# Optimization experiments

Measured on AMD Instinct MI355X. Metric: run time of the kernel, lower is better.

The kernel has to match this reference:

```python
import jax, jax.numpy as jnp
import numpy as np

N_DOMAINS = 8
LN_EPS = 1e-5


def setup_inputs() -> dict:
    key = jax.random.key(0)
    ks = jax.random.split(key, 4)
    N, D_IN, D_HID, D_OUT = 32768, 256, 1024, 256
    x = jax.random.normal(ks[0], (N, D_IN), dtype=jnp.float32)
    domain_types = jax.random.randint(ks[1], (N,), 0, N_DOMAINS, dtype=jnp.int32)
    # Per-domain MLP parameters (8 independent experts)
    W1 = jax.random.normal(ks[2], (N_DOMAINS, D_IN, D_HID), dtype=jnp.float32) * (1.0 / np.sqrt(D_IN))
    b1 = jnp.zeros((N_DOMAINS, D_HID), dtype=jnp.float32)
    gamma = jnp.ones((N_DOMAINS, D_HID), dtype=jnp.float32)
    beta = jnp.zeros((N_DOMAINS, D_HID), dtype=jnp.float32)
    W2 = jax.random.normal(ks[3], (N_DOMAINS, D_HID, D_OUT), dtype=jnp.float32) * (1.0 / np.sqrt(D_HID))
    b2 = jnp.zeros((N_DOMAINS, D_OUT), dtype=jnp.float32)
    return {"x": x, "domain_types": domain_types, "W1": W1, "b1": b1,
            "gamma": gamma, "beta": beta, "W2": W2, "b2": b2}


def _expert_mlp(x, W1d, b1d, gd, bd, W2d, b2d):
    # Linear -> LayerNorm -> ReLU -> (Dropout: identity at eval) -> Linear
    h = x @ W1d + b1d                       # [N, hid]
    mu = jnp.mean(h, axis=-1, keepdims=True)
    var = jnp.mean(jnp.square(h - mu), axis=-1, keepdims=True)
    h = (h - mu) * jax.lax.rsqrt(var + LN_EPS) * gd + bd
    h = jax.nn.relu(h)
    return h @ W2d + b2d                    # [N, out]


def reference(x, domain_types, W1, b1, gamma, beta, W2, b2):
    # output dim == x.shape[-1] (as in the torch code: zeros(batch, x.shape[-1]))
    out = jnp.zeros((x.shape[0], x.shape[-1]), dtype=x.dtype)
    for d in range(N_DOMAINS):  # small fixed expert loop (static MoE dispatch)
        y = _expert_mlp(x, W1[d], b1[d], gamma[d], beta[d], W2[d], b2[d])
        mask = (domain_types == d)[:, None]
        out = jnp.where(mask, y, out)
    return out
```

## Files before the change

### kernel.cpp

```cpp
#include <hip/hip_runtime.h>
#include <hip/hip_bf16.h>


#define ND 8
#define NROWS 32768
#define DIN 256
#define DHID 1024
#define DOUT 256
#define MPAD 33792
#define NTILES 264

typedef short short8 __attribute__((ext_vector_type(8)));
typedef float floatx4 __attribute__((ext_vector_type(4)));

__device__ __forceinline__ unsigned short f2bf(float f) {
    unsigned u = __builtin_bit_cast(unsigned, f);
    unsigned r = u + 0x7fff + ((u >> 16) & 1);
    return (unsigned short)(r >> 16);
}
__device__ __forceinline__ float bf2f(unsigned short h) {
    unsigned u = ((unsigned)h) << 16;
    return __builtin_bit_cast(float, u);
}

#define GLDS16(gp, lp) __builtin_amdgcn_global_load_lds( \
    (const __attribute__((address_space(1))) void*)(gp), \
    (__attribute__((address_space(3))) void*)(lp), 16, 0, 0)

__global__ void transpose_bf16(const float* __restrict__ in,
                               unsigned short* __restrict__ out,
                               int R, int C, int* __restrict__ cnt) {
    __shared__ float t[32][33];
    const int z = blockIdx.z;
    const int c0 = blockIdx.x * 32, r0 = blockIdx.y * 32;
    const int tx = threadIdx.x & 31, ty = threadIdx.x >> 5;
    if (cnt && blockIdx.x == 0 && blockIdx.y == 0 && z == 0 && threadIdx.x < 16)
        cnt[threadIdx.x] = 0;
    const float* src = in + (size_t)z * R * C;
    unsigned short* dst = out + (size_t)z * R * C;
#pragma unroll
    for (int i = 0; i < 32; i += 8)
        t[ty + i][tx] = src[(size_t)(r0 + ty + i) * C + c0 + tx];
    __syncthreads();
#pragma unroll
    for (int i = 0; i < 32; i += 8)
        dst[(size_t)(c0 + ty + i) * R + r0 + tx] = f2bf(t[tx][ty + i]);
}

__global__ void histo(const int* __restrict__ dt, int* __restrict__ counts) {
    __shared__ int lc[ND];
    if (threadIdx.x < ND) lc[threadIdx.x] = 0;
    __syncthreads();
    int i = blockIdx.x * 256 + threadIdx.x;
    atomicAdd(&lc[dt[i]], 1);
    __syncthreads();
    if (threadIdx.x < ND) atomicAdd(&counts[threadIdx.x], lc[threadIdx.x]);
}

__global__ void make_meta(const int* __restrict__ counts, int* __restrict__ cursors,
                          int2* __restrict__ meta, int* __restrict__ perm) {
    if (threadIdx.x == 0 && blockIdx.x == 0) {
        int off = 0, t = 0;
        for (int d = 0; d < ND; d++) {
            cursors[d] = off;
            int nt = (counts[d] + 127) >> 7;
            for (int i = 0; i < nt; i++) meta[t++] = make_int2(d, off + (i << 7));
            for (int p = off + counts[d]; p < off + (nt << 7); p++) perm[p] = -1;
            off += nt << 7;
        }
        for (; t < NTILES; t++) meta[t] = make_int2(-1, 0);
    }
}

__global__ __launch_bounds__(256)
void assign_pos(const int* __restrict__ dt, int* __restrict__ cursors,
                int* __restrict__ perm, int* __restrict__ pos) {
    __shared__ int lcnt[ND];
    __shared__ int lbase[ND];
    const int tid = threadIdx.x;
    if (tid < ND) lcnt[tid] = 0;
    __syncthreads();
    const int r = blockIdx.x * 256 + tid;
    const int d = dt[r];
    const int myrank = atomicAdd(&lcnt[d], 1);
    __syncthreads();
    if (tid < ND && lcnt[tid] > 0)
        lbase[tid] = atomicAdd(&cursors[tid], lcnt[tid]);
    __syncthreads();
    const int p = lbase[d] + myrank;
    pos[r] = p;
    perm[p] = r;
}

__global__ __launch_bounds__(256)
void copy_rows(const float* __restrict__ x, const int* __restrict__ pos,
               unsigned short* __restrict__ xs) {
    const int tid = threadIdx.x;
    const int lane = tid & 63;
    const int r = blockIdx.x * 4 + (tid >> 6);
    const int p = pos[r];
    float4 v = ((const float4*)(x + (size_t)r * DIN))[lane];
    ushort4 o;
    o.x = f2bf(v.x); o.y = f2bf(v.y); o.z = f2bf(v.z); o.w = f2bf(v.w);
    ((ushort4*)(xs + (size_t)p * DIN))[lane] = o;
}

__global__ __launch_bounds__(512, 2)
void gemm_ln(const unsigned short* __restrict__ A,
             const unsigned short* __restrict__ Bt,
             const float* __restrict__ bias,
             const float* __restrict__ gamma,
             const float* __restrict__ beta,
             const int2* __restrict__ meta,
             unsigned short* __restrict__ H) {
    const int2 md = meta[blockIdx.x >> 1];
    const int dom = md.x;
    if (dom < 0) return;
    const int m0 = md.y + (blockIdx.x & 1) * 64;

    __shared__ unsigned short As[64 * 32];
    __shared__ unsigned short Bs[1024 * 32];
    __shared__ float red_s[64][9];
    __shared__ float red_q[64][9];
    __shared__ float mu_s[64], rs_s[64];

    const int tid = threadIdx.x;
    const int lane = tid & 63;
    const int w = tid >> 6;
    const int c16 = lane & 15;
    const int quad = lane >> 4;

    const unsigned short* Abase = A + (size_t)m0 * DIN;
    const unsigned short* Bbase = Bt + (size_t)dom * DHID * DIN;

    floatx4 acc[4][8];
#pragma unroll
    for (int i = 0; i < 4; i++)
#pragma unroll
        for (int j = 0; j < 8; j++) acc[i][j] = 0.f;

    for (int k0 = 0; k0 < DIN; k0 += 32) {
#pragma unroll
        for (int it = 0; it < 8; ++it) {
            const int c = (w * 8 + it) * 64 + lane;
            const int n = c >> 2, kc = c & 3;
            GLDS16(Bbase + (size_t)n * DIN + k0 + kc * 8, &Bs[(w * 8 + it) * 512]);
        }
        if (w < 4) {
            const int c = w * 64 + lane;
            const int m = c >> 2, kc = c & 3;
            GLDS16(Abase + (size_t)m * DIN + k0 + kc * 8, &As[w * 512]);
        }
        __syncthreads();

        const int kk = quad * 8;
        short8 a[4], b[8];
#pragma unroll
        for (int i = 0; i < 4; i++)
            a[i] = *(const short8*)&As[(i * 16 + c16) * 32 + kk];
#pragma unroll
        for (int j = 0; j < 8; j++)
            b[j] = *(const short8*)&Bs[(w * 128 + j * 16 + c16) * 32 + kk];
#pragma unroll
        for (int i = 0; i < 4; i++)
#pragma unroll
            for (int j = 0; j < 8; j++)
                acc[i][j] = __builtin_amdgcn_mfma_f32_16x16x32_bf16(a[i], b[j], acc[i][j], 0, 0, 0);
        __syncthreads();
    }

    float bv[8];
#pragma unroll
    for (int j = 0; j < 8; j++) bv[j] = bias[dom * DHID + w * 128 + j * 16 + c16];

#pragma unroll
    for (int i = 0; i < 4; i++) {
#pragma unroll
        for (int r = 0; r < 4; r++) {
            float s = 0.f, q = 0.f;
#pragma unroll
            for (int j = 0; j < 8; j++) {
                float v = acc[i][j][r] + bv[j];
                acc[i][j][r] = v;
                s += v; q += v * v;
            }
#pragma unroll
            for (int o = 1; o < 16; o <<= 1) {
                s += __shfl_xor(s, o, 64);
                q += __shfl_xor(q, o, 64);
            }
            if (c16 == 0) {
                const int row = i * 16 + quad * 4 + r;
                red_s[row][w] = s;
                red_q[row][w] = q;
            }
        }
    }
    __syncthreads();

    if (tid < 64) {
        float s = 0.f, q = 0.f;
#pragma unroll
        for (int ww = 0; ww < 8; ww++) { s += red_s[tid][ww]; q += red_q[tid][ww]; }
        const float inv = 1.0f / (float)DHID;
        const float mu = s * inv;
        const float var = fmaxf(q * inv - mu * mu, 0.f);
        mu_s[tid] = mu;
        rs_s[tid] = rsqrtf(var + 1e-5f);
    }
    __syncthreads();

    float gv[8], btv[8];
#pragma unroll
    for (int j = 0; j < 8; j++) {
        gv[j] = gamma[dom * DHID + w * 128 + j * 16 + c16];
        btv[j] = beta[dom * DHID + w * 128 + j * 16 + c16];
    }
#pragma unroll
    for (int i = 0; i < 4; i++) {
#pragma unroll
        for (int r = 0; r < 4; r++) {
            const int row = i * 16 + quad * 4 + r;
            const float mu = mu_s[row], rs = rs_s[row];
            unsigned short* hrow = H + (size_t)(m0 + row) * DHID + w * 128;
#pragma unroll
            for (int j = 0; j < 8; j++) {
                float v = (acc[i][j][r] - mu) * rs * gv[j] + btv[j];
                hrow[j * 16 + c16] = f2bf(fmaxf(v, 0.f));
            }
        }
    }
}

__global__ __launch_bounds__(256, 2)
void gemm_bt(const unsigned short* __restrict__ A,
             const unsigned short* __restrict__ Bt,
             const float* __restrict__ bias,
             const int2* __restrict__ meta,
             const int* __restrict__ perm,
             float* __restrict__ Cf,
             const int Ntot, const int K) {
    const int2 md = meta[blockIdx.x];
    const int dom = md.x;
    if (dom < 0) return;
    const int m0 = md.y;
    const int n0 = blockIdx.y * 128;

    __shared__ unsigned short As[128 * 32];
    __shared__ unsigned short Bs[128 * 32];

    const int tid = threadIdx.x;
    const int lane = tid & 63;
    const int w = tid >> 6;
    const int wr = w >> 1, wc = w & 1;

    const unsigned short* Abase = A + (size_t)m0 * K;
    const unsigned short* Bbase = Bt + (size_t)dom * Ntot * K + (size_t)n0 * K;

    floatx4 acc[4][4];
#pragma unroll
    for (int i = 0; i < 4; i++)
#pragma unroll
        for (int j = 0; j < 4; j++) acc[i][j] = 0.f;

    for (int k0 = 0; k0 < K; k0 += 32) {
#pragma unroll
        for (int it = 0; it < 2; ++it) {
            const int c = w * 128 + it * 64 + lane;
            const int m = c >> 2, kc = c & 3;
            GLDS16(Abase + (size_t)m * K + k0 + kc * 8, &As[(w * 128 + it * 64) * 8]);
            GLDS16(Bbase + (size_t)m * K + k0 + kc * 8, &Bs[(w * 128 + it * 64) * 8]);
        }
        __syncthreads();

        short8 a[4], b[4];
        const int kk = (lane >> 4) * 8;
#pragma unroll
        for (int i = 0; i < 4; i++) {
            const int m = wr * 64 + i * 16 + (lane & 15);
            a[i] = *(const short8*)&As[m * 32 + kk];
            const int n = wc * 64 + i * 16 + (lane & 15);
            b[i] = *(const short8*)&Bs[n * 32 + kk];
        }
#pragma unroll
        for (int i = 0; i < 4; i++)
#pragma unroll
            for (int j = 0; j < 4; j++)
                acc[i][j] = __builtin_amdgcn_mfma_f32_16x16x32_bf16(a[i], b[j], acc[i][j], 0, 0, 0);
        __syncthreads();
    }

    const int quad = lane >> 4;
#pragma unroll
    for (int i = 0; i < 4; i++) {
        const int rowbase = m0 + wr * 64 + i * 16 + quad * 4;
#pragma unroll
        for (int r = 0; r < 4; r++) {
            const int orig = perm[rowbase + r];
            if (orig < 0) continue;
#pragma unroll
            for (int j = 0; j < 4; j++) {
                const int col = n0 + wc * 64 + j * 16 + (lane & 15);
                Cf[(size_t)orig * Ntot + col] = acc[i][j][r] + bias[dom * Ntot + col];
            }
        }
    }
}

extern "C" void kernel_launch(void* const* d_in, const int* in_sizes, int n_in,
                              void* d_out, int out_size, void* d_ws, size_t ws_size,
                              hipStream_t stream) {
    const float* x = (const float*)d_in[0];
    const int* dt = (const int*)d_in[1];
    const float* W1 = (const float*)d_in[2];
    const float* b1 = (const float*)d_in[3];
    const float* gamma = (const float*)d_in[4];
    const float* beta = (const float*)d_in[5];
    const float* W2 = (const float*)d_in[6];
    const float* b2 = (const float*)d_in[7];
    float* out = (float*)d_out;

    char* ws = (char*)d_ws;
    size_t off = 0;
    auto take = [&](size_t nbytes) -> char* {
        char* p = ws + off;
        off = (off + nbytes + 255) & ~(size_t)255;
        return p;
    };
    unsigned short* W1T = (unsigned short*)take((size_t)ND * DHID * DIN * 2);
    unsigned short* W2T = (unsigned short*)take((size_t)ND * DOUT * DHID * 2);
    unsigned short* XS  = (unsigned short*)take((size_t)MPAD * DIN * 2);
    unsigned short* H   = (unsigned short*)take((size_t)MPAD * DHID * 2);
    int* PERM   = (int*)take(MPAD * 4);
    int* POS    = (int*)take(NROWS * 4);
    int* CNT    = (int*)take(64);
    int2* META  = (int2*)take(NTILES * 8);
    (void)ws_size; (void)n_in; (void)in_sizes; (void)out_size;

    int* COUNTS = CNT;
    int* CURSORS = CNT + 8;

    transpose_bf16<<<dim3(DHID / 32, DIN / 32, ND), 256, 0, stream>>>(W1, W1T, DIN, DHID, CNT);
    transpose_bf16<<<dim3(DOUT / 32, DHID / 32, ND), 256, 0, stream>>>(W2, W2T, DHID, DOUT, nullptr);
    histo<<<NROWS / 256, 256, 0, stream>>>(dt, COUNTS);
    make_meta<<<1, 1, 0, stream>>>(COUNTS, CURSORS, META, PERM);
    assign_pos<<<NROWS / 256, 256, 0, stream>>>(dt, CURSORS, PERM, POS);
    copy_rows<<<NROWS / 4, 256, 0, stream>>>(x, POS, XS);
    gemm_ln<<<NTILES * 2, 512, 0, stream>>>(XS, W1T, b1, gamma, beta, META, H);
    gemm_bt<<<dim3(NTILES, DOUT / 128), 256, 0, stream>>>(
        H, W2T, b2, META, PERM, out, DOUT, DHID);
}
```

Before: 247.8 us.

## Split LayerNorm: emit partial stats in GEMM1, apply normalization in GEMM2 A-load

The first GEMM used to own full 1024-wide rows (a 64x1024 tile per block with a large LDS B buffer) so it could compute LayerNorm in-block. It now uses standard 128x128 tiles that write pre-norm bf16 H plus per-row partial sums and sums of squares to a stats buffer. The second GEMM reduces those 16 partials per row, then normalizes, applies gamma/beta and ReLU while staging H into LDS. This is meant to give GEMM1 more parallelism and a smaller LDS footprint. In exchange, GEMM2's A path changes from async global-to-LDS loads to register loads with ALU work, and each GEMM2 column block redoes the normalization of the same H rows.

Result: faster. 229.2 us (-7.5%).

```diff
diff --git a/kernel.cpp b/kernel.cpp
--- a/kernel.cpp
+++ b/kernel.cpp
@@ -11,6 +11,7 @@
 #define NTILES 264
 
 typedef short short8 __attribute__((ext_vector_type(8)));
+typedef unsigned short ushort8v __attribute__((ext_vector_type(8)));
 typedef float floatx4 __attribute__((ext_vector_type(4)));
 
 __device__ __forceinline__ unsigned short f2bf(float f) {
@@ -105,83 +106,79 @@
     ((ushort4*)(xs + (size_t)p * DIN))[lane] = o;
 }
 
-__global__ __launch_bounds__(512, 2)
-void gemm_ln(const unsigned short* __restrict__ A,
-             const unsigned short* __restrict__ Bt,
-             const float* __restrict__ bias,
-             const float* __restrict__ gamma,
-             const float* __restrict__ beta,
-             const int2* __restrict__ meta,
-             unsigned short* __restrict__ H) {
-    const int2 md = meta[blockIdx.x >> 1];
+__global__ __launch_bounds__(256, 2)
+void gemm_a(const unsigned short* __restrict__ A,
+            const unsigned short* __restrict__ Bt,
+            const float* __restrict__ bias,
+            const int2* __restrict__ meta,
+            unsigned short* __restrict__ H,
+            float2* __restrict__ stats) {
+    const int2 md = meta[blockIdx.x];
     const int dom = md.x;
     if (dom < 0) return;
-    const int m0 = md.y + (blockIdx.x & 1) * 64;
-
-    __shared__ unsigned short As[64 * 32];
-    __shared__ unsigned short Bs[1024 * 32];
-    __shared__ float red_s[64][9];
-    __shared__ float red_q[64][9];
-    __shared__ float mu_s[64], rs_s[64];
+    const int m0 = md.y;
+    const int n0 = blockIdx.y * 128;
+
+    __shared__ unsigned short As[128 * 32];
+    __shared__ unsigned short Bs[128 * 32];
 
     const int tid = threadIdx.x;
     const int lane = tid & 63;
     const int w = tid >> 6;
-    const int c16 = lane & 15;
-    const int quad = lane >> 4;
+    const int wr = w >> 1, wc = w & 1;
+    const int c16 = lane & 15, quad = lane >> 4;
 
     const unsigned short* Abase = A + (size_t)m0 * DIN;
-    const unsigned short* Bbase = Bt + (size_t)dom * DHID * DIN;
-
-    floatx4 acc[4][8];
+    const unsigned short* Bbase = Bt + (size_t)dom * DHID * DIN + (size_t)n0 * DIN;
+
+    floatx4 acc[4][4];
 #pragma unroll
     for (int i = 0; i < 4; i++)
 #pragma unroll
-        for (int j = 0; j < 8; j++) acc[i][j] = 0.f;
+        for (int j = 0; j < 4; j++) acc[i][j] = 0.f;
 
     for (int k0 = 0; k0 < DIN; k0 += 32) {
 #pragma unroll
-        for (int it = 0; it < 8; ++it) {
-            const int c = (w * 8 + it) * 64 + lane;
-            const int n = c >> 2, kc = c & 3;
-            GLDS16(Bbase + (size_t)n * DIN + k0 + kc * 8, &Bs[(w * 8 + it) * 512]);
-        }
-        if (w < 4) {
-            const int c = w * 64 + lane;
+        for (int it = 0; it < 2; ++it) {
+            const int c = w * 128 + it * 64 + lane;
             const int m = c >> 2, kc = c & 3;
-            GLDS16(Abase + (size_t)m * DIN + k0 + kc * 8, &As[w * 512]);
+            GLDS16(Abase + (size_t)m * DIN + k0 + kc * 8, &As[(w * 128 + it * 64) * 8]);
+            GLDS16(Bbase + (size_t)m * DIN + k0 + kc * 8, &Bs[(w * 128 + it * 64) * 8]);
         }
         __syncthreads();
 
+        short8 a[4], b[4];
         const int kk = quad * 8;
-        short8 a[4], b[8];
+#pragma unroll
+        for (int i = 0; i < 4; i++) {
+            a[i] = *(const short8*)&As[(wr * 64 + i * 16 + c16) * 32 + kk];
+            b[i] = *(const short8*)&Bs[(wc * 64 + i * 16 + c16) * 32 + kk];
+        }
 #pragma unroll
         for (int i = 0; i < 4; i++)
-            a[i] = *(const short8*)&As[(i * 16 + c16) * 32 + kk];
-#pragma unroll
-        for (int j = 0; j < 8; j++)
-            b[j] = *(const short8*)&Bs[(w * 128 + j * 16 + c16) * 32 + kk];
-#pragma unroll
-        for (int i = 0; i < 4; i++)
-#pragma unroll
-            for (int j = 0; j < 8; j++)
+#pragma unroll
+            for (int j = 0; j < 4; j++)
                 acc[i][j] = __builtin_amdgcn_mfma_f32_16x16x32_bf16(a[i], b[j], acc[i][j], 0, 0, 0);
         __syncthreads();
     }
 
-    float bv[8];
-#pragma unroll
-    for (int j = 0; j < 8; j++) bv[j] = bias[dom * DHID + w * 128 + j * 16 + c16];
-
+    float bv[4];
+#pragma unroll
+    for (int j = 0; j < 4; j++)
+        bv[j] = bias[dom * DHID + n0 + wc * 64 + j * 16 + c16];
+
+    float2* st = stats + (size_t)(blockIdx.y * 2 + wc) * MPAD;
 #pragma unroll
     for (int i = 0; i < 4; i++) {
+        const int rowbase = m0 + wr * 64 + i * 16 + quad * 4;
 #pragma unroll
         for (int r = 0; r < 4; r++) {
             float s = 0.f, q = 0.f;
 #pragma unroll
-            for (int j = 0; j < 8; j++) {
-                float v = acc[i][j][r] + bv[j];
-                acc[i][j][r] = v;
+            for (int j = 0; j < 4; j++) {
+                const float v = acc[i][j][r] + bv[j];
+                const int col = n0 + wc * 64 + j * 16 + c16;
+                H[(size_t)(rowbase + r) * DHID + col] = f2bf(v);
                 s += v; q += v * v;
             }
 #pragma unroll
@@ -189,19 +186,44 @@
                 s += __shfl_xor(s, o, 64);
                 q += __shfl_xor(q, o, 64);
             }
-            if (c16 == 0) {
-                const int row = i * 16 + quad * 4 + r;
-                red_s[row][w] = s;
-                red_q[row][w] = q;
-            }
-        }
-    }
-    __syncthreads();
-
-    if (tid < 64) {
+            if (c16 == 0) st[rowbase + r] = make_float2(s, q);
+        }
+    }
+}
+
+__global__ __launch_bounds__(256, 2)
+void gemm_b_ln(const unsigned short* __restrict__ H,
+               const unsigned short* __restrict__ Bt,
+               const float* __restrict__ bias,
+               const float* __restrict__ gamma,
+               const float* __restrict__ beta,
+               const float2* __restrict__ stats,
+               const int2* __restrict__ meta,
+               const int* __restrict__ perm,
+               float* __restrict__ out) {
+    const int2 md = meta[blockIdx.x];
+    const int dom = md.x;
+    if (dom < 0) return;
+    const int m0 = md.y;
+    const int n0 = blockIdx.y * 128;
+
+    __shared__ unsigned short As[128 * 32];
+    __shared__ unsigned short Bs[128 * 32];
+    __shared__ float mu_s[128], rs_s[128];
+
+    const int tid = threadIdx.x;
+    const int lane = tid & 63;
+    const int w = tid >> 6;
+    const int wr = w >> 1, wc = w & 1;
+    const int c16 = lane & 15, quad = lane >> 4;
+
+    if (tid < 128) {
         float s = 0.f, q = 0.f;
 #pragma unroll
-        for (int ww = 0; ww < 8; ww++) { s += red_s[tid][ww]; q += red_q[tid][ww]; }
+        for (int cb = 0; cb < 16; cb++) {
+            const float2 p = stats[(size_t)cb * MPAD + m0 + tid];
+            s += p.x; q += p.y;
+        }
         const float inv = 1.0f / (float)DHID;
         const float mu = s * inv;
         const float var = fmaxf(q * inv - mu * mu, 0.f);
@@ -210,77 +232,52 @@
     }
     __syncthreads();
 
-    float gv[8], btv[8];
-#pragma unroll
-    for (int j = 0; j < 8; j++) {
-        gv[j] = gamma[dom * DHID + w * 128 + j * 16 + c16];
-        btv[j] = beta[dom * DHID + w * 128 + j * 16 + c16];
-    }
-#pragma unroll
-    for (int i = 0; i < 4; i++) {
-#pragma unroll
-        for (int r = 0; r < 4; r++) {
-            const int row = i * 16 + quad * 4 + r;
+    const unsigned short* Hbase = H + (size_t)m0 * DHID;
+    const unsigned short* Bbase = Bt + (size_t)dom * DOUT * DHID + (size_t)n0 * DHID;
+    const float* gbase = gamma + dom * DHID;
+    const float* bbase = beta + dom * DHID;
+
+    floatx4 acc[4][4];
+#pragma unroll
+    for (int i = 0; i < 4; i++)
+#pragma unroll
+        for (int j = 0; j < 4; j++) acc[i][j] = 0.f;
+
+    for (int k0 = 0; k0 < DHID; k0 += 32) {
+#pragma unroll
+        for (int it = 0; it < 2; ++it) {
+            const int c = it * 256 + tid;
+            const int row = c >> 2, kg = c & 3;
             const float mu = mu_s[row], rs = rs_s[row];
-            unsigned short* hrow = H + (size_t)(m0 + row) * DHID + w * 128;
-#pragma unroll
-            for (int j = 0; j < 8; j++) {
-                float v = (acc[i][j][r] - mu) * rs * gv[j] + btv[j];
-                hrow[j * 16 + c16] = f2bf(fmaxf(v, 0.f));
+            const ushort8v hv = *(const ushort8v*)(Hbase + (size_t)row * DHID + k0 + kg * 8);
+            const float4 g0 = *(const float4*)(gbase + k0 + kg * 8);
+            const float4 g1 = *(const float4*)(gbase + k0 + kg * 8 + 4);
+            const float4 b0 = *(const float4*)(bbase + k0 + kg * 8);
+            const float4 b1 = *(const float4*)(bbase + k0 + kg * 8 + 4);
+            float gg[8] = {g0.x, g0.y, g0.z, g0.w, g1.x, g1.y, g1.z, g1.w};
+            float bb[8] = {b0.x, b0.y, b0.z, b0.w, b1.x, b1.y, b1.z, b1.w};
+            ushort8v o;
+#pragma unroll
+            for (int e = 0; e < 8; e++) {
+                const float v = (bf2f(hv[e]) - mu) * rs;
+                o[e] = f2bf(fmaxf(v * gg[e] + bb[e], 0.f));
             }
-        }
-    }
-}
-
-__global__ __launch_bounds__(256, 2)
-void gemm_bt(const unsigned short* __restrict__ A,
-             const unsigned short* __restrict__ Bt,
-             const float* __restrict__ bias,
-             const int2* __restrict__ meta,
-             const int* __restrict__ perm,
-             float* __restrict__ Cf,
-             const int Ntot, const int K) {
-    const int2 md = meta[blockIdx.x];
-    const int dom = md.x;
-    if (dom < 0) return;
-    const int m0 = md.y;
-    const int n0 = blockIdx.y * 128;
-
-    __shared__ unsigned short As[128 * 32];
-    __shared__ unsigned short Bs[128 * 32];
-
-    const int tid = threadIdx.x;
-    const int lane = tid & 63;
-    const int w = tid >> 6;
-    const int wr = w >> 1, wc = w & 1;
-
-    const unsigned short* Abase = A + (size_t)m0 * K;
-    const unsigned short* Bbase = Bt + (size_t)dom * Ntot * K + (size_t)n0 * K;
-
-    floatx4 acc[4][4];
-#pragma unroll
-    for (int i = 0; i < 4; i++)
-#pragma unroll
-        for (int j = 0; j < 4; j++) acc[i][j] = 0.f;
-
-    for (int k0 = 0; k0 < K; k0 += 32) {
+            *(ushort8v*)&As[row * 32 + kg * 8] = o;
+        }
 #pragma unroll
         for (int it = 0; it < 2; ++it) {
             const int c = w * 128 + it * 64 + lane;
             const int m = c >> 2, kc = c & 3;
-            GLDS16(Abase + (size_t)m * K + k0 + kc * 8, &As[(w * 128 + it * 64) * 8]);
-            GLDS16(Bbase + (size_t)m * K + k0 + kc * 8, &Bs[(w * 128 + it * 64) * 8]);
+            GLDS16(Bbase + (size_t)m * DHID + k0 + kc * 8, &Bs[(w * 128 + it * 64) * 8]);
         }
         __syncthreads();
 
         short8 a[4], b[4];
-        const int kk = (lane >> 4) * 8;
+        const int kk = quad * 8;
 #pragma unroll
         for (int i = 0; i < 4; i++) {
-            const int m = wr * 64 + i * 16 + (lane & 15);
-            a[i] = *(const short8*)&As[m * 32 + kk];
-            const int n = wc * 64 + i * 16 + (lane & 15);
-            b[i] = *(const short8*)&Bs[n * 32 + kk];
+            a[i] = *(const short8*)&As[(wr * 64 + i * 16 + c16) * 32 + kk];
+            b[i] = *(const short8*)&Bs[(wc * 64 + i * 16 + c16) * 32 + kk];
         }
 #pragma unroll
         for (int i = 0; i < 4; i++)
@@ -290,7 +287,6 @@
         __syncthreads();
     }
 
-    const int quad = lane >> 4;
 #pragma unroll
     for (int i = 0; i < 4; i++) {
         const int rowbase = m0 + wr * 64 + i * 16 + quad * 4;
@@ -300,8 +296,8 @@
             if (orig < 0) continue;
 #pragma unroll
             for (int j = 0; j < 4; j++) {
-                const int col = n0 + wc * 64 + j * 16 + (lane & 15);
-                Cf[(size_t)orig * Ntot + col] = acc[i][j][r] + bias[dom * Ntot + col];
+                const int col = n0 + wc * 64 + j * 16 + c16;
+                out[(size_t)orig * DOUT + col] = acc[i][j][r] + bias[dom * DOUT + col];
             }
         }
     }
@@ -331,6 +327,7 @@
     unsigned short* W2T = (unsigned short*)take((size_t)ND * DOUT * DHID * 2);
     unsigned short* XS  = (unsigned short*)take((size_t)MPAD * DIN * 2);
     unsigned short* H   = (unsigned short*)take((size_t)MPAD * DHID * 2);
+    float2* STATS = (float2*)take((size_t)16 * MPAD * 8);
     int* PERM   = (int*)take(MPAD * 4);
     int* POS    = (int*)take(NROWS * 4);
     int* CNT    = (int*)take(64);
@@ -346,7 +343,7 @@
     make_meta<<<1, 1, 0, stream>>>(COUNTS, CURSORS, META, PERM);
     assign_pos<<<NROWS / 256, 256, 0, stream>>>(dt, CURSORS, PERM, POS);
     copy_rows<<<NROWS / 4, 256, 0, stream>>>(x, POS, XS);
-    gemm_ln<<<NTILES * 2, 512, 0, stream>>>(XS, W1T, b1, gamma, beta, META, H);
-    gemm_bt<<<dim3(NTILES, DOUT / 128), 256, 0, stream>>>(
-        H, W2T, b2, META, PERM, out, DOUT, DHID);
-}
+    gemm_a<<<dim3(NTILES, DHID / 128), 256, 0, stream>>>(XS, W1T, b1, META, H, STATS);
+    gemm_b_ln<<<dim3(NTILES, DOUT / 128), 256, 0, stream>>>(
+        H, W2T, b2, gamma, beta, STATS, META, PERM, out);
+}
```
